# Optimization experiments

Hardware: AMD Instinct MI355X
Metric: run time of the kernel (lower is better)

The kernel has to match this reference:

```python
import jax, jax.numpy as jnp
import numpy as np

HEADS = 4
DIM_HEAD = 32
GROUPS = 32  # min(256//4, 32)
EPS = 1e-5


def setup_inputs() -> dict:
    key = jax.random.key(0)
    ks = jax.random.split(key, 5)
    B, C, H, W = 16, 256, 64, 64
    CD, HC, WC = 512, 32, 32
    hid = HEADS * DIM_HEAD  # 128
    return {
        "x": jax.random.normal(ks[0], (B, C, H, W), jnp.float32),
        "cond": jax.random.normal(ks[1], (B, CD, HC, WC), jnp.float32),
        "gn_w": jnp.ones((C,), jnp.float32),
        "gn_b": jnp.zeros((C,), jnp.float32),
        "w_q": jax.random.normal(ks[2], (hid, C), jnp.float32) * 0.05,
        "b_q": jnp.zeros((hid,), jnp.float32),
        "w_kv": jax.random.normal(ks[3], (2 * hid, CD), jnp.float32) * 0.05,
        "b_kv": jnp.zeros((2 * hid,), jnp.float32),
        "w_out": jax.random.normal(ks[4], (C, hid), jnp.float32) * 0.05,
        "b_out": jnp.zeros((C,), jnp.float32),
    }


def _group_norm(x, w, b):
    # x: (B, C, H, W); normalize per group over (channels-in-group, H, W)
    B, C, H, W = x.shape
    xg = x.reshape(B, GROUPS, C // GROUPS, H, W)
    mu = jnp.mean(xg, axis=(2, 3, 4), keepdims=True)
    var = jnp.var(xg, axis=(2, 3, 4), keepdims=True)
    xn = ((xg - mu) * jax.lax.rsqrt(var + EPS)).reshape(B, C, H, W)
    return xn * w[None, :, None, None] + b[None, :, None, None]


def _conv1x1(x, w, b):
    # x: (B, Cin, H, W), w: (Cout, Cin), b: (Cout,)
    return jnp.einsum('oc,bchw->bohw', w, x) + b[None, :, None, None]


def reference(x, cond, gn_w, gn_b, w_q, b_q, w_kv, b_kv, w_out, b_out):
    B, C, H, W = x.shape
    hid = HEADS * DIM_HEAD
    xn = _group_norm(x, gn_w, gn_b)
    q = _conv1x1(xn, w_q, b_q)          # (B, hid, H, W)
    kv = _conv1x1(cond, w_kv, b_kv)     # (B, 2*hid, Hc, Wc)
    Nc = kv.shape[2] * kv.shape[3]
    N = H * W
    k = kv[:, :hid].reshape(B, HEADS, DIM_HEAD, Nc)
    v = kv[:, hid:].reshape(B, HEADS, DIM_HEAD, Nc)
    q = q.reshape(B, HEADS, DIM_HEAD, N)
    k = jax.nn.softmax(k, axis=-1)
    # kv outer product: (B, heads, d, e)
    context = jnp.einsum('bhdn,bhen->bhde', k, v)
    # query contraction over d: (B, heads, e, n)
    out = jnp.einsum('bhde,bhdn->bhen', context, q)
    out = out.reshape(B, hid, H, W)
    return _conv1x1(out, w_out, b_out)
```

## Files before the change

kernel.cpp:

```cpp
#include <hip/hip_runtime.h>
#include <hip/hip_bf16.h>

typedef __attribute__((ext_vector_type(8))) short bf16x8;
typedef __attribute__((ext_vector_type(4))) float f32x4;

__device__ __forceinline__ ushort f2bf(float f) {
    __hip_bfloat16 h = __float2bfloat16(f);
    return __builtin_bit_cast(ushort, h);
}
__device__ __forceinline__ unsigned pack2(float a, float b) {
    return (unsigned)f2bf(a) | ((unsigned)f2bf(b) << 16);
}
__device__ __forceinline__ float bflo(unsigned u) { return __uint_as_float(u << 16); }
__device__ __forceinline__ float bfhi(unsigned u) { return __uint_as_float(u & 0xffff0000u); }

__device__ __forceinline__ void unpack8(uint4 r, float* o) {
    o[0] = bflo(r.x); o[1] = bfhi(r.x); o[2] = bflo(r.y); o[3] = bfhi(r.y);
    o[4] = bflo(r.z); o[5] = bfhi(r.z); o[6] = bflo(r.w); o[7] = bfhi(r.w);
}

__global__ __launch_bounds__(256) void kvprep_kernel(const float* __restrict__ w_kv,
                                                     const float* __restrict__ cond,
                                                     const float* __restrict__ b_kv,
                                                     ushort* __restrict__ kv16,
                                                     const float* __restrict__ x,
                                                     float* __restrict__ statacc,
                                                     float* __restrict__ zbase) {
    __shared__ ushort lA[128 * 64];
    __shared__ ushort lB[64 * 64];
    __shared__ float scratch[64 * 64];
    __shared__ float red[8];
    int bid = blockIdx.x, t = threadIdx.x;
    if (bid < 512) {
        int nb = bid & 15, ob = (bid >> 4) & 1, b = bid >> 5;
        int col0 = nb * 64, row0 = ob * 128;
        int l = t & 63, wid = t >> 6;
        int wr = wid >> 1, wc = wid & 1;
        int lr = l & 15, lg = l >> 4;
        const float* Ab32 = w_kv + (size_t)row0 * 512;
        const float* Bb = cond + (size_t)b * 512 * 1024 + col0;
        int sp = t & 31, sj = t >> 5;
        int rA = t >> 3, gAr = t & 7, gw = gAr ^ (rA & 7);
        int rB = t >> 4, gB = t & 15;
        float4 ka0_, ka1_, ka2_, ka3_, ka4_, ka5_, ka6_, ka7_;
        float4 kb0_, kb1_, kb2_, kb3_;
#define KP_LOADA(k0) { \
    ka0_ = *(const float4*)&Ab32[(size_t)(rA)      * 512 + (k0) + gAr * 8]; \
    ka1_ = *(const float4*)&Ab32[(size_t)(rA)      * 512 + (k0) + gAr * 8 + 4]; \
    ka2_ = *(const float4*)&Ab32[(size_t)(32 + rA) * 512 + (k0) + gAr * 8]; \
    ka3_ = *(const float4*)&Ab32[(size_t)(32 + rA) * 512 + (k0) + gAr * 8 + 4]; \
    ka4_ = *(const float4*)&Ab32[(size_t)(64 + rA) * 512 + (k0) + gAr * 8]; \
    ka5_ = *(const float4*)&Ab32[(size_t)(64 + rA) * 512 + (k0) + gAr * 8 + 4]; \
    ka6_ = *(const float4*)&Ab32[(size_t)(96 + rA) * 512 + (k0) + gAr * 8]; \
    ka7_ = *(const float4*)&Ab32[(size_t)(96 + rA) * 512 + (k0) + gAr * 8 + 4]; }
#define KP_LOADB(k0) { \
    kb0_ = *(const float4*)&Bb[(size_t)((k0) + rB)      * 1024 + gB * 4]; \
    kb1_ = *(const float4*)&Bb[(size_t)((k0) + 16 + rB) * 1024 + gB * 4]; \
    kb2_ = *(const float4*)&Bb[(size_t)((k0) + 32 + rB) * 1024 + gB * 4]; \
    kb3_ = *(const float4*)&Bb[(size_t)((k0) + 48 + rB) * 1024 + gB * 4]; }
#define KP_WRITEA() { \
    uint4 p; \
    p.x = pack2(ka0_.x, ka0_.y); p.y = pack2(ka0_.z, ka0_.w); \
    p.z = pack2(ka1_.x, ka1_.y); p.w = pack2(ka1_.z, ka1_.w); \
    *(uint4*)((char*)lA + (size_t)((rA)      * 8 + gw) * 16) = p; \
    p.x = pack2(ka2_.x, ka2_.y); p.y = pack2(ka2_.z, ka2_.w); \
    p.z = pack2(ka3_.x, ka3_.y); p.w = pack2(ka3_.z, ka3_.w); \
    *(uint4*)((char*)lA + (size_t)((32 + rA) * 8 + gw) * 16) = p; \
    p.x = pack2(ka4_.x, ka4_.y); p.y = pack2(ka4_.z, ka4_.w); \
    p.z = pack2(ka5_.x, ka5_.y); p.w = pack2(ka5_.z, ka5_.w); \
    *(uint4*)((char*)lA + (size_t)((64 + rA) * 8 + gw) * 16) = p; \
    p.x = pack2(ka6_.x, ka6_.y); p.y = pack2(ka6_.z, ka6_.w); \
    p.z = pack2(ka7_.x, ka7_.y); p.w = pack2(ka7_.z, ka7_.w); \
    *(uint4*)((char*)lA + (size_t)((96 + rA) * 8 + gw) * 16) = p; }
#define KP_WRITEB() { \
    *(float4*)((char*)scratch + (rB)      * 256 + (gB ^ (((rB)      >> 1) & 15)) * 16) = kb0_; \
    *(float4*)((char*)scratch + (16 + rB) * 256 + (gB ^ (((16 + rB) >> 1) & 15)) * 16) = kb1_; \
    *(float4*)((char*)scratch + (32 + rB) * 256 + (gB ^ (((32 + rB) >> 1) & 15)) * 16) = kb2_; \
    *(float4*)((char*)scratch + (48 + rB) * 256 + (gB ^ (((48 + rB) >> 1) & 15)) * 16) = kb3_; }
#define KP_PACKB() { \
    int swz = sp & 15; \
    float4 s0 = *(const float4*)((char*)scratch + (2*sp)   * 256 + ((2*sj)   ^ swz) * 16); \
    float4 s1 = *(const float4*)((char*)scratch + (2*sp)   * 256 + ((2*sj+1) ^ swz) * 16); \
    float4 s2 = *(const float4*)((char*)scratch + (2*sp+1) * 256 + ((2*sj)   ^ swz) * 16); \
    float4 s3 = *(const float4*)((char*)scratch + (2*sp+1) * 256 + ((2*sj+1) ^ swz) * 16); \
    float c0v[8] = {s0.x, s0.y, s0.z, s0.w, s1.x, s1.y, s1.z, s1.w}; \
    float c1v[8] = {s2.x, s2.y, s2.z, s2.w, s3.x, s3.y, s3.z, s3.w}; \
    _Pragma("unroll") \
    for (int w = 0; w < 8; ++w) { \
        int n = sj * 8 + w; \
        unsigned pk = pack2(c0v[w], c1v[w]); \
        *(unsigned*)((char*)lB + n * 128 + (((sp >> 2) ^ (n & 7)) * 16) + (sp & 3) * 4) = pk; \
    } }
        KP_LOADA(0); KP_LOADB(0);
        f32x4 acc[4][2] = {};
        for (int it = 0; it < 8; ++it) {
            KP_WRITEA();
            KP_WRITEB();
            __syncthreads();
            if (it < 7) { KP_LOADA(it * 64 + 64); KP_LOADB(it * 64 + 64); }
            KP_PACKB();
            __syncthreads();
            #pragma unroll
            for (int ks = 0; ks < 2; ++ks) {
                bf16x8 av[4], bv[2];
                #pragma unroll
                for (int mi = 0; mi < 4; ++mi) {
                    int ar = wr * 64 + mi * 16 + lr;
                    int q = (ks * 4 + lg) ^ (ar & 7);
                    av[mi] = *(const bf16x8*)((const char*)lA + ar * 128 + q * 16);
                }
                #pragma unroll
                for (int ni = 0; ni < 2; ++ni) {
                    int br = wc * 32 + ni * 16 + lr;
                    int q = (ks * 4 + lg) ^ (br & 7);
                    bv[ni] = *(const bf16x8*)((const char*)lB + br * 128 + q * 16);
                }
                #pragma unroll
                for (int mi = 0; mi < 4; ++mi)
                    #pragma unroll
                    for (int ni = 0; ni < 2; ++ni)
                        acc[mi][ni] = __builtin_amdgcn_mfma_f32_16x16x32_bf16(
                            av[mi], bv[ni], acc[mi][ni], 0, 0, 0);
            }
            __syncthreads();
        }
#undef KP_LOADA
#undef KP_LOADB
#undef KP_WRITEA
#undef KP_WRITEB
#undef KP_PACKB
        int orow = row0 + wr * 64, ocol = col0 + wc * 32 + lr;
        #pragma unroll
        for (int mi = 0; mi < 4; ++mi) {
            int rb = orow + mi * 16 + lg * 4;
            float4 b4 = *(const float4*)&b_kv[rb];
            float bvr[4] = {b4.x, b4.y, b4.z, b4.w};
            #pragma unroll
            for (int ni = 0; ni < 2; ++ni) {
                int cc = ocol + ni * 16;
                #pragma unroll
                for (int r = 0; r < 4; ++r)
                    kv16[((size_t)b * 256 + rb + r) * 1024 + cc] = f2bf(acc[mi][ni][r] + bvr[r]);
            }
        }
    } else {
        int bg = bid - 512;
        int zi = bg * 256 + t;
        if (zi < 67584) zbase[zi] = 0.f;
        const float4* xp = (const float4*)(x + (size_t)bg * 32768);
        float s = 0.f, ss = 0.f;
        #pragma unroll
        for (int j = 0; j < 32; ++j) {
            float4 v = xp[t + 256 * j];
            s  += v.x + v.y + v.z + v.w;
            ss += v.x*v.x + v.y*v.y + v.z*v.z + v.w*v.w;
        }
        #pragma unroll
        for (int off = 32; off > 0; off >>= 1) {
            s  += __shfl_down(s, off, 64);
            ss += __shfl_down(ss, off, 64);
        }
        int wave = t >> 6;
        if ((t & 63) == 0) { red[wave * 2] = s; red[wave * 2 + 1] = ss; }
        __syncthreads();
        if (t == 0) {
            statacc[bg * 2]     = red[0] + red[2] + red[4] + red[6];
            statacc[bg * 2 + 1] = red[1] + red[3] + red[5] + red[7];
        }
    }
}

__global__ __launch_bounds__(256) void ctx_partial_kernel(const ushort* __restrict__ kv,
                                                          float* __restrict__ rowsum,
                                                          float* __restrict__ ctx) {
    int bh = blockIdx.y, b = bh >> 2, h = bh & 3;
    int n0 = blockIdx.x * 128;
    __shared__ float pl[32][129], vl[32][129];
    int t = threadIdx.x;
    int r = t >> 3, cs = (t & 7) * 16;
    const ushort* kp = kv + ((size_t)b * 256 + h * 32 + r) * 1024 + n0 + cs;
    const ushort* vp = kv + ((size_t)b * 256 + 128 + h * 32 + r) * 1024 + n0 + cs;
    float kvals[16], vvals[16];
    unpack8(((const uint4*)kp)[0], kvals);
    unpack8(((const uint4*)kp)[1], kvals + 8);
    unpack8(((const uint4*)vp)[0], vvals);
    unpack8(((const uint4*)vp)[1], vvals + 8);
    float psum = 0.f;
    #pragma unroll
    for (int i = 0; i < 16; ++i) {
        float e = __expf(kvals[i]);
        pl[r][cs + i] = e;
        vl[r][cs + i] = vvals[i];
        psum += e;
    }
    psum += __shfl_xor(psum, 1, 64);
    psum += __shfl_xor(psum, 2, 64);
    psum += __shfl_xor(psum, 4, 64);
    if ((t & 7) == 0) atomicAdd(&rowsum[bh * 32 + r], psum);
    __syncthreads();
    int d0 = t >> 5, e0 = t & 31;
    float acc[4] = {0.f, 0.f, 0.f, 0.f};
    #pragma unroll 8
    for (int nn = 0; nn < 128; ++nn) {
        float vv = vl[e0][nn];
        #pragma unroll
        for (int i = 0; i < 4; ++i)
            acc[i] += pl[d0 + 8 * i][nn] * vv;
    }
    #pragma unroll
    for (int i = 0; i < 4; ++i)
        atomicAdd(&ctx[((size_t)bh * 32 + d0 + 8 * i) * 32 + e0], acc[i]);
}

__global__ __launch_bounds__(256) void a_kernel(const float* __restrict__ ctx,
                                                const float* __restrict__ rowsum,
                                                const float* __restrict__ w_out,
                                                const float* __restrict__ w_q,
                                                const float* __restrict__ b_q,
                                                const float* __restrict__ statacc,
                                                const float* __restrict__ gn_w,
                                                const float* __restrict__ gn_b,
                                                const float* __restrict__ b_out,
                                                ushort* __restrict__ A16,
                                                float* __restrict__ biasb) {
    __shared__ float ctxl[4][32][33];
    __shared__ float wol[16][128];
    __shared__ float ml[16][128];
    __shared__ float cbuf[256][17];
    __shared__ float pbuf[16][17];
    int b = blockIdx.x >> 4, ot = (blockIdx.x & 15) << 4;
    int t = threadIdx.x;
    #pragma unroll
    for (int j = 0; j < 16; ++j) {
        int e = t + 256 * j;
        float inv = 1.f / rowsum[b * 128 + (e >> 5)];
        ctxl[e >> 10][(e >> 5) & 31][e & 31] = ctx[(size_t)b * 4096 + e] * inv;
    }
    #pragma unroll
    for (int j = 0; j < 8; ++j) {
        int e = t + 256 * j;
        wol[e >> 7][e & 127] = w_out[(ot + (e >> 7)) * 128 + (e & 127)];
    }
    __syncthreads();
    #pragma unroll
    for (int j = 0; j < 8; ++j) {
        int e = t + 256 * j;
        int o = e >> 7, hd = e & 127, h = hd >> 5, d = hd & 31;
        float acc = 0.f;
        #pragma unroll
        for (int ee = 0; ee < 32; ++ee) acc += wol[o][h * 32 + ee] * ctxl[h][d][ee];
        ml[o][hd] = acc;
    }
    __syncthreads();
    int c = t, g = c >> 3;
    float a0 = statacc[(b * 32 + g) * 2], a1 = statacc[(b * 32 + g) * 2 + 1];
    float mu  = a0 * (1.f / 32768.f);
    float var = a1 * (1.f / 32768.f) - mu * mu;
    float sc = rsqrtf(var + 1e-5f) * gn_w[c];
    float tc = gn_b[c] - mu * sc;
    float wt[16];
    #pragma unroll
    for (int o = 0; o < 16; ++o) wt[o] = 0.f;
    for (int hd = 0; hd < 128; ++hd) {
        float wq = w_q[hd * 256 + c];
        #pragma unroll
        for (int o = 0; o < 16; ++o) wt[o] += ml[o][hd] * wq;
    }
    ushort* Abp = A16 + ((size_t)b * 256 + ot) * 256 + c;
    #pragma unroll
    for (int o = 0; o < 16; ++o) {
        Abp[(size_t)o * 256] = f2bf(wt[o] * sc);
        cbuf[c][o] = wt[o] * tc;
    }
    __syncthreads();
    {
        int o = t >> 4, seg = t & 15;
        float p = 0.f;
        #pragma unroll
        for (int i = 0; i < 16; ++i) p += cbuf[seg * 16 + i][o];
        pbuf[o][seg] = p;
    }
    __syncthreads();
    if (t < 16) {
        int o = t;
        float sum = 0.f;
        #pragma unroll
        for (int s2 = 0; s2 < 16; ++s2) sum += pbuf[o][s2];
        float md = 0.f;
        #pragma unroll 8
        for (int hd = 0; hd < 128; ++hd) md += ml[o][hd] * b_q[hd];
        biasb[(size_t)b * 256 + ot + o] = sum + md + b_out[ot + o];
    }
}

__global__ __launch_bounds__(512) void out_gemm_fused(const ushort* __restrict__ A16,
                                                      const float* __restrict__ x,
                                                      const float* __restrict__ biasb,
                                                      float* __restrict__ out) {
    __shared__ ushort lA[256 * 64];
    __shared__ ushort lB[128 * 64];
    __shared__ float scratch[64 * 128];
    int b = blockIdx.y;
    int n0 = blockIdx.x * 128;
    int t = threadIdx.x;
    int l = t & 63, wid = t >> 6;
    int wr = wid >> 1, wc = wid & 1;
    int lr = l & 15, lg = l >> 4;
    const ushort* Ab = A16 + (size_t)b * 65536;
    const float* xb = x + (size_t)b * 256 * 4096 + n0;
    int sp = t & 31, sj = t >> 5;
    uint4 a0_, a1_, a2_, a3_;
    float4 b0_, b1_, b2_, b3_;
    int rA = t >> 3, gA = (t & 7) ^ (rA & 7);
    int rB = t >> 5, gB = t & 31;
#define OG_LOADA(k0) { \
    a0_ = *(const uint4*)(Ab + (size_t)(rA)       * 256 + (k0) + gA * 8); \
    a1_ = *(const uint4*)(Ab + (size_t)(64 + rA)  * 256 + (k0) + gA * 8); \
    a2_ = *(const uint4*)(Ab + (size_t)(128 + rA) * 256 + (k0) + gA * 8); \
    a3_ = *(const uint4*)(Ab + (size_t)(192 + rA) * 256 + (k0) + gA * 8); }
#define OG_LOADB(k0) { \
    b0_ = *(const float4*)&xb[(size_t)((k0) + rB)      * 4096 + gB * 4]; \
    b1_ = *(const float4*)&xb[(size_t)((k0) + 16 + rB) * 4096 + gB * 4]; \
    b2_ = *(const float4*)&xb[(size_t)((k0) + 32 + rB) * 4096 + gB * 4]; \
    b3_ = *(const float4*)&xb[(size_t)((k0) + 48 + rB) * 4096 + gB * 4]; }
    OG_LOADA(0); OG_LOADB(0);
    f32x4 acc[4][4] = {};
    for (int it = 0; it < 4; ++it) {
        *(uint4*)((char*)lA + (size_t)t * 16)          = a0_;
        *(uint4*)((char*)lA + (size_t)(512 + t) * 16)  = a1_;
        *(uint4*)((char*)lA + (size_t)(1024 + t) * 16) = a2_;
        *(uint4*)((char*)lA + (size_t)(1536 + t) * 16) = a3_;
        *(float4*)((char*)scratch + (rB)      * 512 + (gB ^ (((rB)      >> 1) & 31)) * 16) = b0_;
        *(float4*)((char*)scratch + (16 + rB) * 512 + (gB ^ (((16 + rB) >> 1) & 31)) * 16) = b1_;
        *(float4*)((char*)scratch + (32 + rB) * 512 + (gB ^ (((32 + rB) >> 1) & 31)) * 16) = b2_;
        *(float4*)((char*)scratch + (48 + rB) * 512 + (gB ^ (((48 + rB) >> 1) & 31)) * 16) = b3_;
        __syncthreads();
        if (it < 3) { OG_LOADA(it * 64 + 64); OG_LOADB(it * 64 + 64); }
        {
            int swz = sp & 31;
            float4 s0 = *(const float4*)((char*)scratch + (2*sp)   * 512 + ((2*sj)   ^ swz) * 16);
            float4 s1 = *(const float4*)((char*)scratch + (2*sp)   * 512 + ((2*sj+1) ^ swz) * 16);
            float4 s2 = *(const float4*)((char*)scratch + (2*sp+1) * 512 + ((2*sj)   ^ swz) * 16);
            float4 s3 = *(const float4*)((char*)scratch + (2*sp+1) * 512 + ((2*sj+1) ^ swz) * 16);
            float c0v[8] = {s0.x, s0.y, s0.z, s0.w, s1.x, s1.y, s1.z, s1.w};
            float c1v[8] = {s2.x, s2.y, s2.z, s2.w, s3.x, s3.y, s3.z, s3.w};
            #pragma unroll
            for (int w = 0; w < 8; ++w) {
                int n = sj * 8 + w;
                unsigned pk = pack2(c0v[w], c1v[w]);
                *(unsigned*)((char*)lB + n * 128 + (((sp >> 2) ^ (n & 7)) * 16) + (sp & 3) * 4) = pk;
            }
        }
        __syncthreads();
        #pragma unroll
        for (int ks = 0; ks < 2; ++ks) {
            bf16x8 av[4], bv[4];
            #pragma unroll
            for (int mi = 0; mi < 4; ++mi) {
                int ar = wr * 64 + mi * 16 + lr;
                int q = (ks * 4 + lg) ^ (ar & 7);
                av[mi] = *(const bf16x8*)((const char*)lA + ar * 128 + q * 16);
            }
            #pragma unroll
            for (int ni = 0; ni < 4; ++ni) {
                int br = wc * 64 + ni * 16 + lr;
                int q = (ks * 4 + lg) ^ (br & 7);
                bv[ni] = *(const bf16x8*)((const char*)lB + br * 128 + q * 16);
            }
            #pragma unroll
            for (int mi = 0; mi < 4; ++mi)
                #pragma unroll
                for (int ni = 0; ni < 4; ++ni)
                    acc[mi][ni] = __builtin_amdgcn_mfma_f32_16x16x32_bf16(
                        av[mi], bv[ni], acc[mi][ni], 0, 0, 0);
        }
        __syncthreads();
    }
#undef OG_LOADA
#undef OG_LOADB
    const float* bp = biasb + (size_t)b * 256;
    int orow = wr * 64, ocol = n0 + wc * 64 + lr;
    #pragma unroll
    for (int mi = 0; mi < 4; ++mi) {
        int rb = orow + mi * 16 + lg * 4;
        float4 b4 = *(const float4*)&bp[rb];
        float bvr[4] = {b4.x, b4.y, b4.z, b4.w};
        #pragma unroll
        for (int ni = 0; ni < 4; ++ni) {
            int cc = ocol + ni * 16;
            #pragma unroll
            for (int r = 0; r < 4; ++r)
                out[((size_t)b * 256 + rb + r) * 4096 + cc] = acc[mi][ni][r] + bvr[r];
        }
    }
}

extern "C" void kernel_launch(void* const* d_in, const int* in_sizes, int n_in,
                              void* d_out, int out_size, void* d_ws, size_t ws_size,
                              hipStream_t stream) {
    const float* x     = (const float*)d_in[0];
    const float* cond  = (const float*)d_in[1];
    const float* gn_w  = (const float*)d_in[2];
    const float* gn_b  = (const float*)d_in[3];
    const float* w_q   = (const float*)d_in[4];
    const float* b_q   = (const float*)d_in[5];
    const float* w_kv  = (const float*)d_in[6];
    const float* b_kv  = (const float*)d_in[7];
    const float* w_out = (const float*)d_in[8];
    const float* b_out = (const float*)d_in[9];
    float* out = (float*)d_out;

    float* f       = (float*)d_ws;
    float* statacc = f;
    float* rowsum  = f + 1024;
    float* ctx     = f + 3072;
    float* biasb   = f + 68608;
    ushort* u      = (ushort*)(f + 72704);
    ushort* kv16   = u;
    ushort* A16    = u + 4194304;

    kvprep_kernel<<<1024, 256, 0, stream>>>(w_kv, cond, b_kv, kv16, x, statacc, rowsum);
    ctx_partial_kernel<<<dim3(8, 64), 256, 0, stream>>>(kv16, rowsum, ctx);
    a_kernel<<<256, 256, 0, stream>>>(ctx, rowsum, w_out, w_q, b_q, statacc,
                                      gn_w, gn_b, b_out, A16, biasb);
    out_gemm_fused<<<dim3(32, 16), 512, 0, stream>>>(A16, x, biasb, out);
}
```

Measured before the change: 80.67 us.

## Regroup kernels: smaller KV GEMM tiles, fuse ctx with stats, apply GroupNorm in out GEMM

The KV projection GEMM now uses 128x32 tiles over a 3D grid of 1024 blocks, and it also zeroes the accumulators. The GroupNorm statistics pass moves into the context-partial kernel, so that work shares one launch and can overlap it. The per-channel GroupNorm scale and shift is now applied to x while it is packed to bf16 inside the output GEMM, not folded into the A matrix and bias. This removes the cbuf/pbuf reduction in a_kernel but adds a multiply-add per staged element in the main GEMM.

New measurement: 81.29 us. No clear change (+0.8%).

```diff
diff --git a/kernel.cpp b/kernel.cpp
--- a/kernel.cpp
+++ b/kernel.cpp
@@ -19,32 +19,29 @@
     o[4] = bflo(r.z); o[5] = bfhi(r.z); o[6] = bflo(r.w); o[7] = bfhi(r.w);
 }
 
-__global__ __launch_bounds__(256) void kvprep_kernel(const float* __restrict__ w_kv,
-                                                     const float* __restrict__ cond,
-                                                     const float* __restrict__ b_kv,
-                                                     ushort* __restrict__ kv16,
-                                                     const float* __restrict__ x,
-                                                     float* __restrict__ statacc,
-                                                     float* __restrict__ zbase) {
+__global__ __launch_bounds__(256) void kv_gemm(const float* __restrict__ w_kv,
+                                               const float* __restrict__ cond,
+                                               const float* __restrict__ b_kv,
+                                               ushort* __restrict__ kv16,
+                                               float* __restrict__ zbase) {
     __shared__ ushort lA[128 * 64];
-    __shared__ ushort lB[64 * 64];
-    __shared__ float scratch[64 * 64];
-    __shared__ float red[8];
-    int bid = blockIdx.x, t = threadIdx.x;
-    if (bid < 512) {
-        int nb = bid & 15, ob = (bid >> 4) & 1, b = bid >> 5;
-        int col0 = nb * 64, row0 = ob * 128;
-        int l = t & 63, wid = t >> 6;
-        int wr = wid >> 1, wc = wid & 1;
-        int lr = l & 15, lg = l >> 4;
-        const float* Ab32 = w_kv + (size_t)row0 * 512;
-        const float* Bb = cond + (size_t)b * 512 * 1024 + col0;
-        int sp = t & 31, sj = t >> 5;
-        int rA = t >> 3, gAr = t & 7, gw = gAr ^ (rA & 7);
-        int rB = t >> 4, gB = t & 15;
-        float4 ka0_, ka1_, ka2_, ka3_, ka4_, ka5_, ka6_, ka7_;
-        float4 kb0_, kb1_, kb2_, kb3_;
-#define KP_LOADA(k0) { \
+    __shared__ ushort lB[32 * 64];
+    __shared__ float scratch[64 * 32];
+    int nc = blockIdx.x, rb = blockIdx.y, b = blockIdx.z;
+    int t = threadIdx.x;
+    int fid = blockIdx.x + 32 * (blockIdx.y + 2 * blockIdx.z);
+    if (fid < 264) zbase[fid * 256 + t] = 0.f;
+    int col0 = nc * 32, row0 = rb * 128;
+    int l = t & 63, w = t >> 6;
+    int lr = l & 15, lg = l >> 4;
+    const float* Ab32 = w_kv + (size_t)row0 * 512;
+    const float* Bb = cond + (size_t)b * 512 * 1024 + col0;
+    int rA = t >> 3, gAr = t & 7, gw = gAr ^ (rA & 7);
+    int rB = t >> 3, gB = t & 7;
+    int sp = t & 31, sj4 = (t >> 5) & 7;
+    float4 ka0_, ka1_, ka2_, ka3_, ka4_, ka5_, ka6_, ka7_;
+    float4 kb0_, kb1_;
+#define KG_LOADA(k0) { \
     ka0_ = *(const float4*)&Ab32[(size_t)(rA)      * 512 + (k0) + gAr * 8]; \
     ka1_ = *(const float4*)&Ab32[(size_t)(rA)      * 512 + (k0) + gAr * 8 + 4]; \
     ka2_ = *(const float4*)&Ab32[(size_t)(32 + rA) * 512 + (k0) + gAr * 8]; \
@@ -53,13 +50,10 @@
     ka5_ = *(const float4*)&Ab32[(size_t)(64 + rA) * 512 + (k0) + gAr * 8 + 4]; \
     ka6_ = *(const float4*)&Ab32[(size_t)(96 + rA) * 512 + (k0) + gAr * 8]; \
     ka7_ = *(const float4*)&Ab32[(size_t)(96 + rA) * 512 + (k0) + gAr * 8 + 4]; }
-#define KP_LOADB(k0) { \
+#define KG_LOADB(k0) { \
     kb0_ = *(const float4*)&Bb[(size_t)((k0) + rB)      * 1024 + gB * 4]; \
-    kb1_ = *(const float4*)&Bb[(size_t)((k0) + 16 + rB) * 1024 + gB * 4]; \
-    kb2_ = *(const float4*)&Bb[(size_t)((k0) + 32 + rB) * 1024 + gB * 4]; \
-    kb3_ = *(const float4*)&Bb[(size_t)((k0) + 48 + rB) * 1024 + gB * 4]; }
-#define KP_WRITEA() { \
-    uint4 p; \
+    kb1_ = *(const float4*)&Bb[(size_t)((k0) + 32 + rB) * 1024 + gB * 4]; }
+#define KG_WRITEA() { uint4 p; \
     p.x = pack2(ka0_.x, ka0_.y); p.y = pack2(ka0_.z, ka0_.w); \
     p.z = pack2(ka1_.x, ka1_.y); p.w = pack2(ka1_.z, ka1_.w); \
     *(uint4*)((char*)lA + (size_t)((rA)      * 8 + gw) * 16) = p; \
@@ -72,81 +66,120 @@
     p.x = pack2(ka6_.x, ka6_.y); p.y = pack2(ka6_.z, ka6_.w); \
     p.z = pack2(ka7_.x, ka7_.y); p.w = pack2(ka7_.z, ka7_.w); \
     *(uint4*)((char*)lA + (size_t)((96 + rA) * 8 + gw) * 16) = p; }
-#define KP_WRITEB() { \
-    *(float4*)((char*)scratch + (rB)      * 256 + (gB ^ (((rB)      >> 1) & 15)) * 16) = kb0_; \
-    *(float4*)((char*)scratch + (16 + rB) * 256 + (gB ^ (((16 + rB) >> 1) & 15)) * 16) = kb1_; \
-    *(float4*)((char*)scratch + (32 + rB) * 256 + (gB ^ (((32 + rB) >> 1) & 15)) * 16) = kb2_; \
-    *(float4*)((char*)scratch + (48 + rB) * 256 + (gB ^ (((48 + rB) >> 1) & 15)) * 16) = kb3_; }
-#define KP_PACKB() { \
-    int swz = sp & 15; \
-    float4 s0 = *(const float4*)((char*)scratch + (2*sp)   * 256 + ((2*sj)   ^ swz) * 16); \
-    float4 s1 = *(const float4*)((char*)scratch + (2*sp)   * 256 + ((2*sj+1) ^ swz) * 16); \
-    float4 s2 = *(const float4*)((char*)scratch + (2*sp+1) * 256 + ((2*sj)   ^ swz) * 16); \
-    float4 s3 = *(const float4*)((char*)scratch + (2*sp+1) * 256 + ((2*sj+1) ^ swz) * 16); \
-    float c0v[8] = {s0.x, s0.y, s0.z, s0.w, s1.x, s1.y, s1.z, s1.w}; \
-    float c1v[8] = {s2.x, s2.y, s2.z, s2.w, s3.x, s3.y, s3.z, s3.w}; \
+#define KG_WRITEB() { \
+    *(float4*)((char*)scratch + (rB)      * 128 + ((gB ^ (((rB)      >> 1) & 7)) * 16)) = kb0_; \
+    *(float4*)((char*)scratch + (32 + rB) * 128 + ((gB ^ (((32 + rB) >> 1) & 7)) * 16)) = kb1_; }
+#define KG_PACKB() { \
+    int js = sj4 ^ (sp & 7); \
+    float4 s0 = *(const float4*)((char*)scratch + (2*sp)   * 128 + js * 16); \
+    float4 s2 = *(const float4*)((char*)scratch + (2*sp+1) * 128 + js * 16); \
+    float c0v[4] = {s0.x, s0.y, s0.z, s0.w}; \
+    float c1v[4] = {s2.x, s2.y, s2.z, s2.w}; \
     _Pragma("unroll") \
-    for (int w = 0; w < 8; ++w) { \
-        int n = sj * 8 + w; \
-        unsigned pk = pack2(c0v[w], c1v[w]); \
+    for (int w4 = 0; w4 < 4; ++w4) { \
+        int n = sj4 * 4 + w4; \
+        unsigned pk = pack2(c0v[w4], c1v[w4]); \
         *(unsigned*)((char*)lB + n * 128 + (((sp >> 2) ^ (n & 7)) * 16) + (sp & 3) * 4) = pk; \
     } }
-        KP_LOADA(0); KP_LOADB(0);
-        f32x4 acc[4][2] = {};
-        for (int it = 0; it < 8; ++it) {
-            KP_WRITEA();
-            KP_WRITEB();
-            __syncthreads();
-            if (it < 7) { KP_LOADA(it * 64 + 64); KP_LOADB(it * 64 + 64); }
-            KP_PACKB();
-            __syncthreads();
-            #pragma unroll
-            for (int ks = 0; ks < 2; ++ks) {
-                bf16x8 av[4], bv[2];
+    KG_LOADA(0); KG_LOADB(0);
+    f32x4 acc[2][2] = {};
+    for (int it = 0; it < 8; ++it) {
+        KG_WRITEA();
+        KG_WRITEB();
+        __syncthreads();
+        if (it < 7) { KG_LOADA(it * 64 + 64); KG_LOADB(it * 64 + 64); }
+        KG_PACKB();
+        __syncthreads();
+        #pragma unroll
+        for (int ks = 0; ks < 2; ++ks) {
+            bf16x8 av[2], bv[2];
+            #pragma unroll
+            for (int mi = 0; mi < 2; ++mi) {
+                int ar = w * 32 + mi * 16 + lr;
+                int q = (ks * 4 + lg) ^ (ar & 7);
+                av[mi] = *(const bf16x8*)((const char*)lA + ar * 128 + q * 16);
+            }
+            #pragma unroll
+            for (int ni = 0; ni < 2; ++ni) {
+                int br = ni * 16 + lr;
+                int q = (ks * 4 + lg) ^ (br & 7);
+                bv[ni] = *(const bf16x8*)((const char*)lB + br * 128 + q * 16);
+            }
+            #pragma unroll
+            for (int mi = 0; mi < 2; ++mi)
                 #pragma unroll
-                for (int mi = 0; mi < 4; ++mi) {
-                    int ar = wr * 64 + mi * 16 + lr;
-                    int q = (ks * 4 + lg) ^ (ar & 7);
-                    av[mi] = *(const bf16x8*)((const char*)lA + ar * 128 + q * 16);
-                }
-                #pragma unroll
-                for (int ni = 0; ni < 2; ++ni) {
-                    int br = wc * 32 + ni * 16 + lr;
-                    int q = (ks * 4 + lg) ^ (br & 7);
-                    bv[ni] = *(const bf16x8*)((const char*)lB + br * 128 + q * 16);
-                }
-                #pragma unroll
-                for (int mi = 0; mi < 4; ++mi)
-                    #pragma unroll
-                    for (int ni = 0; ni < 2; ++ni)
-                        acc[mi][ni] = __builtin_amdgcn_mfma_f32_16x16x32_bf16(
-                            av[mi], bv[ni], acc[mi][ni], 0, 0, 0);
-            }
-            __syncthreads();
-        }
-#undef KP_LOADA
-#undef KP_LOADB
-#undef KP_WRITEA
-#undef KP_WRITEB
-#undef KP_PACKB
-        int orow = row0 + wr * 64, ocol = col0 + wc * 32 + lr;
-        #pragma unroll
-        for (int mi = 0; mi < 4; ++mi) {
-            int rb = orow + mi * 16 + lg * 4;
-            float4 b4 = *(const float4*)&b_kv[rb];
-            float bvr[4] = {b4.x, b4.y, b4.z, b4.w};
-            #pragma unroll
-            for (int ni = 0; ni < 2; ++ni) {
-                int cc = ocol + ni * 16;
-                #pragma unroll
-                for (int r = 0; r < 4; ++r)
-                    kv16[((size_t)b * 256 + rb + r) * 1024 + cc] = f2bf(acc[mi][ni][r] + bvr[r]);
-            }
-        }
+                for (int ni = 0; ni < 2; ++ni)
+                    acc[mi][ni] = __builtin_amdgcn_mfma_f32_16x16x32_bf16(
+                        av[mi], bv[ni], acc[mi][ni], 0, 0, 0);
+        }
+        __syncthreads();
+    }
+#undef KG_LOADA
+#undef KG_LOADB
+#undef KG_WRITEA
+#undef KG_WRITEB
+#undef KG_PACKB
+    int orow = row0 + w * 32;
+    #pragma unroll
+    for (int mi = 0; mi < 2; ++mi) {
+        int rbase = orow + mi * 16 + lg * 4;
+        float4 b4 = *(const float4*)&b_kv[rbase];
+        float bvr[4] = {b4.x, b4.y, b4.z, b4.w};
+        #pragma unroll
+        for (int ni = 0; ni < 2; ++ni) {
+            int cc = col0 + ni * 16 + lr;
+            #pragma unroll
+            for (int r = 0; r < 4; ++r)
+                kv16[((size_t)b * 256 + rbase + r) * 1024 + cc] = f2bf(acc[mi][ni][r] + bvr[r]);
+        }
+    }
+}
+
+__global__ __launch_bounds__(256) void ctxstats_kernel(const ushort* __restrict__ kv,
+                                                       const float* __restrict__ x,
+                                                       float* __restrict__ rowsum,
+                                                       float* __restrict__ ctx,
+                                                       float* __restrict__ statacc) {
+    __shared__ float pl[32][129], vl[32][129];
+    int bid = blockIdx.x, t = threadIdx.x;
+    if (bid < 512) {
+        int bh = bid >> 3, b = bh >> 2, h = bh & 3;
+        int n0 = (bid & 7) * 128;
+        int r = t >> 3, cs = (t & 7) * 16;
+        const ushort* kp = kv + ((size_t)b * 256 + h * 32 + r) * 1024 + n0 + cs;
+        const ushort* vp = kv + ((size_t)b * 256 + 128 + h * 32 + r) * 1024 + n0 + cs;
+        float kvals[16], vvals[16];
+        unpack8(((const uint4*)kp)[0], kvals);
+        unpack8(((const uint4*)kp)[1], kvals + 8);
+        unpack8(((const uint4*)vp)[0], vvals);
+        unpack8(((const uint4*)vp)[1], vvals + 8);
+        float psum = 0.f;
+        #pragma unroll
+        for (int i = 0; i < 16; ++i) {
+            float e = __expf(kvals[i]);
+            pl[r][cs + i] = e;
+            vl[r][cs + i] = vvals[i];
+            psum += e;
+        }
+        psum += __shfl_xor(psum, 1, 64);
+        psum += __shfl_xor(psum, 2, 64);
+        psum += __shfl_xor(psum, 4, 64);
+        if ((t & 7) == 0) atomicAdd(&rowsum[bh * 32 + r], psum);
+        __syncthreads();
+        int d0 = t >> 5, e0 = t & 31;
+        float acc[4] = {0.f, 0.f, 0.f, 0.f};
+        #pragma unroll 8
+        for (int nn = 0; nn < 128; ++nn) {
+            float vv = vl[e0][nn];
+            #pragma unroll
+            for (int i = 0; i < 4; ++i)
+                acc[i] += pl[d0 + 8 * i][nn] * vv;
+        }
+        #pragma unroll
+        for (int i = 0; i < 4; ++i)
+            atomicAdd(&ctx[((size_t)bh * 32 + d0 + 8 * i) * 32 + e0], acc[i]);
     } else {
         int bg = bid - 512;
-        int zi = bg * 256 + t;
-        if (zi < 67584) zbase[zi] = 0.f;
         const float4* xp = (const float4*)(x + (size_t)bg * 32768);
         float s = 0.f, ss = 0.f;
         #pragma unroll
@@ -161,55 +194,13 @@
             ss += __shfl_down(ss, off, 64);
         }
         int wave = t >> 6;
-        if ((t & 63) == 0) { red[wave * 2] = s; red[wave * 2 + 1] = ss; }
+        if ((t & 63) == 0) { pl[0][wave * 2] = s; pl[0][wave * 2 + 1] = ss; }
         __syncthreads();
         if (t == 0) {
-            statacc[bg * 2]     = red[0] + red[2] + red[4] + red[6];
-            statacc[bg * 2 + 1] = red[1] + red[3] + red[5] + red[7];
-        }
-    }
-}
-
-__global__ __launch_bounds__(256) void ctx_partial_kernel(const ushort* __restrict__ kv,
-                                                          float* __restrict__ rowsum,
-                                                          float* __restrict__ ctx) {
-    int bh = blockIdx.y, b = bh >> 2, h = bh & 3;
-    int n0 = blockIdx.x * 128;
-    __shared__ float pl[32][129], vl[32][129];
-    int t = threadIdx.x;
-    int r = t >> 3, cs = (t & 7) * 16;
-    const ushort* kp = kv + ((size_t)b * 256 + h * 32 + r) * 1024 + n0 + cs;
-    const ushort* vp = kv + ((size_t)b * 256 + 128 + h * 32 + r) * 1024 + n0 + cs;
-    float kvals[16], vvals[16];
-    unpack8(((const uint4*)kp)[0], kvals);
-    unpack8(((const uint4*)kp)[1], kvals + 8);
-    unpack8(((const uint4*)vp)[0], vvals);
-    unpack8(((const uint4*)vp)[1], vvals + 8);
-    float psum = 0.f;
-    #pragma unroll
-    for (int i = 0; i < 16; ++i) {
-        float e = __expf(kvals[i]);
-        pl[r][cs + i] = e;
-        vl[r][cs + i] = vvals[i];
-        psum += e;
-    }
-    psum += __shfl_xor(psum, 1, 64);
-    psum += __shfl_xor(psum, 2, 64);
-    psum += __shfl_xor(psum, 4, 64);
-    if ((t & 7) == 0) atomicAdd(&rowsum[bh * 32 + r], psum);
-    __syncthreads();
-    int d0 = t >> 5, e0 = t & 31;
-    float acc[4] = {0.f, 0.f, 0.f, 0.f};
-    #pragma unroll 8
-    for (int nn = 0; nn < 128; ++nn) {
-        float vv = vl[e0][nn];
-        #pragma unroll
-        for (int i = 0; i < 4; ++i)
-            acc[i] += pl[d0 + 8 * i][nn] * vv;
-    }
-    #pragma unroll
-    for (int i = 0; i < 4; ++i)
-        atomicAdd(&ctx[((size_t)bh * 32 + d0 + 8 * i) * 32 + e0], acc[i]);
+            statacc[bg * 2]     = pl[0][0] + pl[0][2] + pl[0][4] + pl[0][6];
+            statacc[bg * 2 + 1] = pl[0][1] + pl[0][3] + pl[0][5] + pl[0][7];
+        }
+    }
 }
 
 __global__ __launch_bounds__(256) void a_kernel(const float* __restrict__ ctx,
@@ -217,17 +208,12 @@
                                                 const float* __restrict__ w_out,
                                                 const float* __restrict__ w_q,
                                                 const float* __restrict__ b_q,
-                                                const float* __restrict__ statacc,
-                                                const float* __restrict__ gn_w,
-                                                const float* __restrict__ gn_b,
                                                 const float* __restrict__ b_out,
                                                 ushort* __restrict__ A16,
                                                 float* __restrict__ biasb) {
     __shared__ float ctxl[4][32][33];
     __shared__ float wol[16][128];
     __shared__ float ml[16][128];
-    __shared__ float cbuf[256][17];
-    __shared__ float pbuf[16][17];
     int b = blockIdx.x >> 4, ot = (blockIdx.x & 15) << 4;
     int t = threadIdx.x;
     #pragma unroll
@@ -252,12 +238,7 @@
         ml[o][hd] = acc;
     }
     __syncthreads();
-    int c = t, g = c >> 3;
-    float a0 = statacc[(b * 32 + g) * 2], a1 = statacc[(b * 32 + g) * 2 + 1];
-    float mu  = a0 * (1.f / 32768.f);
-    float var = a1 * (1.f / 32768.f) - mu * mu;
-    float sc = rsqrtf(var + 1e-5f) * gn_w[c];
-    float tc = gn_b[c] - mu * sc;
+    int c = t;
     float wt[16];
     #pragma unroll
     for (int o = 0; o < 16; ++o) wt[o] = 0.f;
@@ -268,38 +249,28 @@
     }
     ushort* Abp = A16 + ((size_t)b * 256 + ot) * 256 + c;
     #pragma unroll
-    for (int o = 0; o < 16; ++o) {
-        Abp[(size_t)o * 256] = f2bf(wt[o] * sc);
-        cbuf[c][o] = wt[o] * tc;
-    }
-    __syncthreads();
-    {
-        int o = t >> 4, seg = t & 15;
-        float p = 0.f;
-        #pragma unroll
-        for (int i = 0; i < 16; ++i) p += cbuf[seg * 16 + i][o];
-        pbuf[o][seg] = p;
-    }
-    __syncthreads();
+    for (int o = 0; o < 16; ++o)
+        Abp[(size_t)o * 256] = f2bf(wt[o]);
     if (t < 16) {
         int o = t;
-        float sum = 0.f;
-        #pragma unroll
-        for (int s2 = 0; s2 < 16; ++s2) sum += pbuf[o][s2];
         float md = 0.f;
         #pragma unroll 8
         for (int hd = 0; hd < 128; ++hd) md += ml[o][hd] * b_q[hd];
-        biasb[(size_t)b * 256 + ot + o] = sum + md + b_out[ot + o];
+        biasb[(size_t)b * 256 + ot + o] = md + b_out[ot + o];
     }
 }
 
 __global__ __launch_bounds__(512) void out_gemm_fused(const ushort* __restrict__ A16,
                                                       const float* __restrict__ x,
+                                                      const float* __restrict__ statacc,
+                                                      const float* __restrict__ gn_w,
+                                                      const float* __restrict__ gn_b,
                                                       const float* __restrict__ biasb,
                                                       float* __restrict__ out) {
     __shared__ ushort lA[256 * 64];
     __shared__ ushort lB[128 * 64];
     __shared__ float scratch[64 * 128];
+    __shared__ float sct[256][2];
     int b = blockIdx.y;
     int n0 = blockIdx.x * 128;
     int t = threadIdx.x;
@@ -309,6 +280,16 @@
     const ushort* Ab = A16 + (size_t)b * 65536;
     const float* xb = x + (size_t)b * 256 * 4096 + n0;
     int sp = t & 31, sj = t >> 5;
+    if (t < 256) {
+        int g = t >> 3;
+        float S  = statacc[(b * 32 + g) * 2];
+        float SS = statacc[(b * 32 + g) * 2 + 1];
+        float mu  = S * (1.f / 32768.f);
+        float var = SS * (1.f / 32768.f) - mu * mu;
+        float sc = rsqrtf(var + 1e-5f) * gn_w[t];
+        sct[t][0] = sc;
+        sct[t][1] = gn_b[t] - mu * sc;
+    }
     uint4 a0_, a1_, a2_, a3_;
     float4 b0_, b1_, b2_, b3_;
     int rA = t >> 3, gA = (t & 7) ^ (rA & 7);
@@ -326,6 +307,7 @@
     OG_LOADA(0); OG_LOADB(0);
     f32x4 acc[4][4] = {};
     for (int it = 0; it < 4; ++it) {
+        int k0 = it * 64;
         *(uint4*)((char*)lA + (size_t)t * 16)          = a0_;
         *(uint4*)((char*)lA + (size_t)(512 + t) * 16)  = a1_;
         *(uint4*)((char*)lA + (size_t)(1024 + t) * 16) = a2_;
@@ -335,9 +317,11 @@
         *(float4*)((char*)scratch + (32 + rB) * 512 + (gB ^ (((32 + rB) >> 1) & 31)) * 16) = b2_;
         *(float4*)((char*)scratch + (48 + rB) * 512 + (gB ^ (((48 + rB) >> 1) & 31)) * 16) = b3_;
         __syncthreads();
-        if (it < 3) { OG_LOADA(it * 64 + 64); OG_LOADB(it * 64 + 64); }
+        if (it < 3) { OG_LOADA(k0 + 64); OG_LOADB(k0 + 64); }
         {
             int swz = sp & 31;
+            float sc0 = sct[k0 + 2 * sp][0],     tc0 = sct[k0 + 2 * sp][1];
+            float sc1 = sct[k0 + 2 * sp + 1][0], tc1 = sct[k0 + 2 * sp + 1][1];
             float4 s0 = *(const float4*)((char*)scratch + (2*sp)   * 512 + ((2*sj)   ^ swz) * 16);
             float4 s1 = *(const float4*)((char*)scratch + (2*sp)   * 512 + ((2*sj+1) ^ swz) * 16);
             float4 s2 = *(const float4*)((char*)scratch + (2*sp+1) * 512 + ((2*sj)   ^ swz) * 16);
@@ -347,7 +331,7 @@
             #pragma unroll
             for (int w = 0; w < 8; ++w) {
                 int n = sj * 8 + w;
-                unsigned pk = pack2(c0v[w], c1v[w]);
+                unsigned pk = pack2(c0v[w] * sc0 + tc0, c1v[w] * sc1 + tc1);
                 *(unsigned*)((char*)lB + n * 128 + (((sp >> 2) ^ (n & 7)) * 16) + (sp & 3) * 4) = pk;
             }
         }
@@ -419,9 +403,8 @@
     ushort* kv16   = u;
     ushort* A16    = u + 4194304;
 
-    kvprep_kernel<<<1024, 256, 0, stream>>>(w_kv, cond, b_kv, kv16, x, statacc, rowsum);
-    ctx_partial_kernel<<<dim3(8, 64), 256, 0, stream>>>(kv16, rowsum, ctx);
-    a_kernel<<<256, 256, 0, stream>>>(ctx, rowsum, w_out, w_q, b_q, statacc,
-                                      gn_w, gn_b, b_out, A16, biasb);
-    out_gemm_fused<<<dim3(32, 16), 512, 0, stream>>>(A16, x, biasb, out);
-}
+    kv_gemm<<<dim3(32, 2, 16), 256, 0, stream>>>(w_kv, cond, b_kv, kv16, rowsum);
+    ctxstats_kernel<<<1024, 256, 0, stream>>>(kv16, x, rowsum, ctx, statacc);
+    a_kernel<<<256, 256, 0, stream>>>(ctx, rowsum, w_out, w_q, b_q, b_out, A16, biasb);
+    out_gemm_fused<<<dim3(32, 16), 512, 0, stream>>>(A16, x, statacc, gn_w, gn_b, biasb, out);
+}
```
